# Optimization experiments

Hardware: AMD Instinct MI355X
Metric: run time of the kernel (lower is better)

The kernel has to match this reference:

```python
import jax, jax.numpy as jnp
import numpy as np

B, H, S, D = 4, 8, 8192, 64


def setup_inputs() -> dict:
    key = jax.random.key(0)
    kq, kk, kv_, kqm, kkm = jax.random.split(key, 5)
    q = jax.random.normal(kq, (B, H, S, D), dtype=jnp.float32)
    k = jax.random.normal(kk, (B, H, S, D), dtype=jnp.float32)
    v = jax.random.normal(kv_, (B, H, S, D), dtype=jnp.float32)
    q_mask = jax.random.randint(kqm, (B, S), 0, 2).astype(jnp.bool_)
    kv_mask = jax.random.randint(kkm, (B, S), 0, 2).astype(jnp.bool_)
    return {"q": q, "k": k, "v": v, "q_mask": q_mask, "kv_mask": kv_mask}


def reference(q, k, v, q_mask, kv_mask):
    # Linear (kernelized) attention branch: feature map phi(x) = elu(x) + 1
    qe = jax.nn.elu(q) + 1.0
    ke = jax.nn.elu(k) + 1.0
    qm = q_mask.astype(q.dtype)[:, None, :, None]   # [B,1,S,1]
    km = kv_mask.astype(q.dtype)[:, None, :, None]
    qe = qe * qm
    ke = ke * km
    ve = v * km
    s = v.shape[2]
    # kv: [B,H,D,D] contraction over kv sequence
    kv = jnp.einsum('bhsd,bhsc->bhdc', ke, ve / s)
    # normalizer per query position: [B,H,L]
    div = 1.0 / (jnp.einsum('bhld,bhsd->bhl', qe, ke) + 1e-6)
    out = s * jnp.einsum('bhld,bhdc,bhl->bhlc', qe, kv, div)
    return out
```

## Files before the change

kernel.cpp:

```cpp
#include <hip/hip_runtime.h>
#include <hip/hip_bf16.h>


#define S_LEN 8192
#define NBH 32
#define KVSTRIDE 4160

typedef __attribute__((ext_vector_type(8))) short short8;
typedef __attribute__((ext_vector_type(4))) float f32x4;

__device__ __forceinline__ float elu1(float x) {
  return x > 0.0f ? (x + 1.0f) : __expf(x);
}
__device__ __forceinline__ unsigned short f2bf(float x) {
  __hip_bfloat16 h = __float2bfloat16(x);
  union { __hip_bfloat16 b; unsigned short u; } cv; cv.b = h; return cv.u;
}
__device__ __forceinline__ float bf2f(unsigned short u) {
  return __uint_as_float(((unsigned)u) << 16);
}
__device__ __forceinline__ void split2(float x, unsigned short& hi, unsigned short& lo) {
  hi = f2bf(x);
  lo = f2bf(x - bf2f(hi));
}
__device__ __forceinline__ short8 ones8() {
  short8 o;
#pragma unroll
  for (int i = 0; i < 8; ++i) o[i] = (short)0x3F80;
  return o;
}

#define MFMA(a,b,c) __builtin_amdgcn_mfma_f32_16x16x32_bf16((a),(b),(c),0,0,0)

__global__ __launch_bounds__(256) void k1_partial(
    const float* __restrict__ kin, const float* __restrict__ vin,
    const int* __restrict__ kv_mask, float* __restrict__ partials, int seg_rows) {
  __shared__ unsigned short keT_h[64 * 72];
  __shared__ unsigned short keT_l[64 * 72];
  __shared__ unsigned short veT_h[64 * 72];
  __shared__ unsigned short veT_l[64 * 72];
  const int tid = threadIdx.x;
  const int seg = blockIdx.x, bh = blockIdx.y, b = bh >> 3;
  const int dp = tid & 31;
  const int so = tid >> 5;
  const int lane = tid & 63, w = tid >> 6;
  const int mrow = lane & 15, qd4 = lane >> 4;
  const short8 one = ones8();

  f32x4 acc[4]; f32x4 accs;
#pragma unroll
  for (int t = 0; t < 4; ++t) acc[t] = (f32x4){0.f, 0.f, 0.f, 0.f};
  accs = (f32x4){0.f, 0.f, 0.f, 0.f};

  const int rbase = seg * seg_rows;
  for (int t0 = 0; t0 < seg_rows; t0 += 64) {
    const int r0 = rbase + t0;
    const float* kp = kin + ((size_t)bh * S_LEN + r0 + so * 8) * 64 + dp * 2;
    const float* vp = vin + ((size_t)bh * S_LEN + r0 + so * 8) * 64 + dp * 2;
    union { unsigned short u[8]; uint4 v; } kh0, kh1, kl0, kl1, vh0, vh1, vl0, vl1;
#pragma unroll
    for (int r = 0; r < 8; ++r) {
      float m = kv_mask[b * S_LEN + r0 + so * 8 + r] ? 1.0f : 0.0f;
      float2 kw = *(const float2*)(kp + (size_t)r * 64);
      float2 vw = *(const float2*)(vp + (size_t)r * 64);
      float ka = elu1(kw.x) * m;
      float kb = elu1(kw.y) * m;
      float mv = m * (1.0f / 8192.0f);
      float va = vw.x * mv, vb = vw.y * mv;
      split2(ka, kh0.u[r], kl0.u[r]);
      split2(kb, kh1.u[r], kl1.u[r]);
      split2(va, vh0.u[r], vl0.u[r]);
      split2(vb, vh1.u[r], vl1.u[r]);
    }
    const int d0 = dp * 2;
    *(uint4*)&keT_h[(d0    ) * 72 + so * 8] = kh0.v;
    *(uint4*)&keT_h[(d0 + 1) * 72 + so * 8] = kh1.v;
    *(uint4*)&keT_l[(d0    ) * 72 + so * 8] = kl0.v;
    *(uint4*)&keT_l[(d0 + 1) * 72 + so * 8] = kl1.v;
    *(uint4*)&veT_h[(d0    ) * 72 + so * 8] = vh0.v;
    *(uint4*)&veT_h[(d0 + 1) * 72 + so * 8] = vh1.v;
    *(uint4*)&veT_l[(d0    ) * 72 + so * 8] = vl0.v;
    *(uint4*)&veT_l[(d0 + 1) * 72 + so * 8] = vl1.v;
    __syncthreads();
#pragma unroll
    for (int k0 = 0; k0 < 64; k0 += 32) {
      short8 a_h = *(const short8*)&keT_h[(w * 16 + mrow) * 72 + k0 + qd4 * 8];
      short8 a_l = *(const short8*)&keT_l[(w * 16 + mrow) * 72 + k0 + qd4 * 8];
      accs = MFMA(a_h, one, accs);
      accs = MFMA(a_l, one, accs);
#pragma unroll
      for (int t = 0; t < 4; ++t) {
        short8 b_h = *(const short8*)&veT_h[(t * 16 + mrow) * 72 + k0 + qd4 * 8];
        short8 b_l = *(const short8*)&veT_l[(t * 16 + mrow) * 72 + k0 + qd4 * 8];
        acc[t] = MFMA(a_h, b_h, acc[t]);
        acc[t] = MFMA(a_h, b_l, acc[t]);
        acc[t] = MFMA(a_l, b_h, acc[t]);
      }
    }
    __syncthreads();
  }
  float* p = partials + ((size_t)bh * gridDim.x + seg) * KVSTRIDE;
#pragma unroll
  for (int t = 0; t < 4; ++t)
#pragma unroll
    for (int r = 0; r < 4; ++r)
      p[(w * 16 + qd4 * 4 + r) * 64 + t * 16 + mrow] = acc[t][r];
  if (mrow == 0) {
#pragma unroll
    for (int r = 0; r < 4; ++r) p[4096 + w * 16 + qd4 * 4 + r] = accs[r];
  }
}

__global__ __launch_bounds__(256) void k2_reduce(
    const float* __restrict__ partials,
    unsigned short* __restrict__ kvTh, unsigned short* __restrict__ kvTl,
    unsigned short* __restrict__ ksh, unsigned short* __restrict__ ksl, int nchunk) {
  const int idx = blockIdx.x * 256 + threadIdx.x;
  if (idx >= NBH * KVSTRIDE) return;
  const int bh = idx / KVSTRIDE;
  const int e = idx - bh * KVSTRIDE;
  const float* p = partials + (size_t)bh * nchunk * KVSTRIDE + e;
  float s0 = 0.f, s1 = 0.f, s2 = 0.f, s3 = 0.f;
  int c = 0;
  for (; c + 4 <= nchunk; c += 4) {
    s0 += p[(size_t)(c + 0) * KVSTRIDE];
    s1 += p[(size_t)(c + 1) * KVSTRIDE];
    s2 += p[(size_t)(c + 2) * KVSTRIDE];
    s3 += p[(size_t)(c + 3) * KVSTRIDE];
  }
  for (; c < nchunk; ++c) s0 += p[(size_t)c * KVSTRIDE];
  float s = (s0 + s1) + (s2 + s3);
  unsigned short hi, lo;
  split2(s, hi, lo);
  if (e < 4096) {
    int d = e >> 6, cc = e & 63;
    kvTh[(size_t)bh * 4096 + cc * 64 + d] = hi;
    kvTl[(size_t)bh * 4096 + cc * 64 + d] = lo;
  } else {
    int d = e - 4096;
    ksh[bh * 64 + d] = hi;
    ksl[bh * 64 + d] = lo;
  }
}

__global__ __launch_bounds__(256) void k3_out(
    const float* __restrict__ qin, const int* __restrict__ q_mask,
    const unsigned short* __restrict__ kvTh_g, const unsigned short* __restrict__ kvTl_g,
    const unsigned short* __restrict__ ksh_g, const unsigned short* __restrict__ ksl_g,
    float* __restrict__ out) {
  __shared__ unsigned short qe_h[64 * 72];
  __shared__ unsigned short qe_l[64 * 72];
  __shared__ unsigned short kv_h[64 * 72];
  __shared__ unsigned short kv_l[64 * 72];
  __shared__ __align__(16) unsigned short ks_h[64];
  __shared__ __align__(16) unsigned short ks_l[64];
  const int tid = threadIdx.x;
  const int rb = blockIdx.x, bh = blockIdx.y, b = bh >> 3;
  const int r0 = rb * 64;
#pragma unroll
  for (int i = 0; i < 4; ++i) {
    int qd = i * 256 + tid;
    int l = qd >> 4, dq = qd & 15;
    float m = q_mask[b * S_LEN + r0 + l] ? 1.0f : 0.0f;
    float4 qw = *(const float4*)(qin + ((size_t)bh * S_LEN + r0 + l) * 64 + dq * 4);
    union { unsigned short u[4]; uint2 v; } h, lo;
    float e0 = elu1(qw.x) * m, e1 = elu1(qw.y) * m, e2 = elu1(qw.z) * m, e3 = elu1(qw.w) * m;
    split2(e0, h.u[0], lo.u[0]);
    split2(e1, h.u[1], lo.u[1]);
    split2(e2, h.u[2], lo.u[2]);
    split2(e3, h.u[3], lo.u[3]);
    *(uint2*)&qe_h[l * 72 + dq * 4] = h.v;
    *(uint2*)&qe_l[l * 72 + dq * 4] = lo.v;
  }
  for (int e = tid; e < 2048; e += 256) {
    int c = (e * 2) >> 6, d = (e * 2) & 63;
    *(unsigned*)&kv_h[c * 72 + d] = *(const unsigned*)(kvTh_g + (size_t)bh * 4096 + e * 2);
    *(unsigned*)&kv_l[c * 72 + d] = *(const unsigned*)(kvTl_g + (size_t)bh * 4096 + e * 2);
  }
  if (tid < 64) {
    ks_h[tid] = ksh_g[bh * 64 + tid];
    ks_l[tid] = ksl_g[bh * 64 + tid];
  }
  __syncthreads();
  const int lane = tid & 63, w = tid >> 6;
  const int mrow = lane & 15, qd4 = lane >> 4;
  f32x4 acc[4]; f32x4 accd;
#pragma unroll
  for (int t = 0; t < 4; ++t) acc[t] = (f32x4){0.f, 0.f, 0.f, 0.f};
  accd = (f32x4){0.f, 0.f, 0.f, 0.f};
#pragma unroll
  for (int k0 = 0; k0 < 64; k0 += 32) {
    short8 a_h = *(const short8*)&qe_h[(w * 16 + mrow) * 72 + k0 + qd4 * 8];
    short8 a_l = *(const short8*)&qe_l[(w * 16 + mrow) * 72 + k0 + qd4 * 8];
    short8 s_h = *(const short8*)&ks_h[k0 + qd4 * 8];
    short8 s_l = *(const short8*)&ks_l[k0 + qd4 * 8];
    accd = MFMA(a_h, s_h, accd);
    accd = MFMA(a_h, s_l, accd);
    accd = MFMA(a_l, s_h, accd);
#pragma unroll
    for (int t = 0; t < 4; ++t) {
      short8 b_h = *(const short8*)&kv_h[(t * 16 + mrow) * 72 + k0 + qd4 * 8];
      short8 b_l = *(const short8*)&kv_l[(t * 16 + mrow) * 72 + k0 + qd4 * 8];
      acc[t] = MFMA(a_h, b_h, acc[t]);
      acc[t] = MFMA(a_h, b_l, acc[t]);
      acc[t] = MFMA(a_l, b_h, acc[t]);
    }
  }
#pragma unroll
  for (int r = 0; r < 4; ++r) {
    float inv = 8192.0f / (accd[r] + 1e-6f);
    int row = r0 + w * 16 + qd4 * 4 + r;
#pragma unroll
    for (int t = 0; t < 4; ++t)
      out[((size_t)bh * S_LEN + row) * 64 + t * 16 + mrow] = acc[t][r] * inv;
  }
}

extern "C" void kernel_launch(void* const* d_in, const int* in_sizes, int n_in,
                              void* d_out, int out_size, void* d_ws, size_t ws_size,
                              hipStream_t stream) {
  const float* q = (const float*)d_in[0];
  const float* k = (const float*)d_in[1];
  const float* v = (const float*)d_in[2];
  const int* qm = (const int*)d_in[3];
  const int* km = (const int*)d_in[4];
  float* out = (float*)d_out;

  int nchunk = 32;
  while (nchunk > 1) {
    size_t need = (size_t)NBH * nchunk * KVSTRIDE * 4
                + (size_t)NBH * 4096 * 2 * 2 + (size_t)NBH * 64 * 2 * 2;
    if (need <= ws_size) break;
    nchunk >>= 1;
  }
  float* partials = (float*)d_ws;
  unsigned short* kvTh = (unsigned short*)(partials + (size_t)NBH * nchunk * KVSTRIDE);
  unsigned short* kvTl = kvTh + (size_t)NBH * 4096;
  unsigned short* ksh  = kvTl + (size_t)NBH * 4096;
  unsigned short* ksl  = ksh + NBH * 64;
  int seg_rows = S_LEN / nchunk;

  k1_partial<<<dim3(nchunk, NBH), 256, 0, stream>>>(k, v, km, partials, seg_rows);
  int n_elem = NBH * KVSTRIDE;
  k2_reduce<<<dim3((n_elem + 255) / 256), 256, 0, stream>>>(partials, kvTh, kvTl, ksh, ksl, nchunk);
  k3_out<<<dim3(S_LEN / 64, NBH), 256, 0, stream>>>(q, qm, kvTh, kvTl, ksh, ksl, out);
}
```

Before: 240.4 us.

## Replace split-bf16 MFMA path with fp32 FMA and register double-buffered loads

The three-way bf16 hi/lo split MFMA emulation of fp32 is dropped in all kernels and replaced by plain fp32 FMA outer products on LDS tiles. k1 gains register double buffering of K/V tiles, computes the key sum with per-thread vector adds, and doubles the chunk count. k2 now writes plain fp32 kv. k3 computes the normalizer with a dot product and an LDS reduction. This removes the conversion and split work and the 3x MFMA count, but the matmuls now run on the vector ALUs instead of the matrix cores.

```diff
diff --git a/kernel.cpp b/kernel.cpp
--- a/kernel.cpp
+++ b/kernel.cpp
@@ -1,120 +1,125 @@
 #include <hip/hip_runtime.h>
-#include <hip/hip_bf16.h>
 
 
 #define S_LEN 8192
 #define NBH 32
 #define KVSTRIDE 4160
 
-typedef __attribute__((ext_vector_type(8))) short short8;
 typedef __attribute__((ext_vector_type(4))) float f32x4;
 
 __device__ __forceinline__ float elu1(float x) {
   return x > 0.0f ? (x + 1.0f) : __expf(x);
 }
-__device__ __forceinline__ unsigned short f2bf(float x) {
-  __hip_bfloat16 h = __float2bfloat16(x);
-  union { __hip_bfloat16 b; unsigned short u; } cv; cv.b = h; return cv.u;
-}
-__device__ __forceinline__ float bf2f(unsigned short u) {
-  return __uint_as_float(((unsigned)u) << 16);
-}
-__device__ __forceinline__ void split2(float x, unsigned short& hi, unsigned short& lo) {
-  hi = f2bf(x);
-  lo = f2bf(x - bf2f(hi));
-}
-__device__ __forceinline__ short8 ones8() {
-  short8 o;
-#pragma unroll
-  for (int i = 0; i < 8; ++i) o[i] = (short)0x3F80;
-  return o;
-}
-
-#define MFMA(a,b,c) __builtin_amdgcn_mfma_f32_16x16x32_bf16((a),(b),(c),0,0,0)
 
 __global__ __launch_bounds__(256) void k1_partial(
     const float* __restrict__ kin, const float* __restrict__ vin,
     const int* __restrict__ kv_mask, float* __restrict__ partials, int seg_rows) {
-  __shared__ unsigned short keT_h[64 * 72];
-  __shared__ unsigned short keT_l[64 * 72];
-  __shared__ unsigned short veT_h[64 * 72];
-  __shared__ unsigned short veT_l[64 * 72];
+  __shared__ float ke_lds[64 * 64];
+  __shared__ float ve_lds[64 * 64];
   const int tid = threadIdx.x;
   const int seg = blockIdx.x, bh = blockIdx.y, b = bh >> 3;
-  const int dp = tid & 31;
-  const int so = tid >> 5;
-  const int lane = tid & 63, w = tid >> 6;
-  const int mrow = lane & 15, qd4 = lane >> 4;
-  const short8 one = ones8();
-
-  f32x4 acc[4]; f32x4 accs;
-#pragma unroll
-  for (int t = 0; t < 4; ++t) acc[t] = (f32x4){0.f, 0.f, 0.f, 0.f};
-  accs = (f32x4){0.f, 0.f, 0.f, 0.f};
-
   const int rbase = seg * seg_rows;
-  for (int t0 = 0; t0 < seg_rows; t0 += 64) {
-    const int r0 = rbase + t0;
-    const float* kp = kin + ((size_t)bh * S_LEN + r0 + so * 8) * 64 + dp * 2;
-    const float* vp = vin + ((size_t)bh * S_LEN + r0 + so * 8) * 64 + dp * 2;
-    union { unsigned short u[8]; uint4 v; } kh0, kh1, kl0, kl1, vh0, vh1, vl0, vl1;
-#pragma unroll
-    for (int r = 0; r < 8; ++r) {
-      float m = kv_mask[b * S_LEN + r0 + so * 8 + r] ? 1.0f : 0.0f;
-      float2 kw = *(const float2*)(kp + (size_t)r * 64);
-      float2 vw = *(const float2*)(vp + (size_t)r * 64);
-      float ka = elu1(kw.x) * m;
-      float kb = elu1(kw.y) * m;
-      float mv = m * (1.0f / 8192.0f);
-      float va = vw.x * mv, vb = vw.y * mv;
-      split2(ka, kh0.u[r], kl0.u[r]);
-      split2(kb, kh1.u[r], kl1.u[r]);
-      split2(va, vh0.u[r], vl0.u[r]);
-      split2(vb, vh1.u[r], vl1.u[r]);
-    }
-    const int d0 = dp * 2;
-    *(uint4*)&keT_h[(d0    ) * 72 + so * 8] = kh0.v;
-    *(uint4*)&keT_h[(d0 + 1) * 72 + so * 8] = kh1.v;
-    *(uint4*)&keT_l[(d0    ) * 72 + so * 8] = kl0.v;
-    *(uint4*)&keT_l[(d0 + 1) * 72 + so * 8] = kl1.v;
-    *(uint4*)&veT_h[(d0    ) * 72 + so * 8] = vh0.v;
-    *(uint4*)&veT_h[(d0 + 1) * 72 + so * 8] = vh1.v;
-    *(uint4*)&veT_l[(d0    ) * 72 + so * 8] = vl0.v;
-    *(uint4*)&veT_l[(d0 + 1) * 72 + so * 8] = vl1.v;
+  const int dg = tid >> 4, cg = tid & 15;
+  const float* kbase = kin + (size_t)bh * S_LEN * 64;
+  const float* vbase = vin + (size_t)bh * S_LEN * 64;
+  const int* mbase = kv_mask + b * S_LEN;
+
+  f32x4 ka[4], va[4], kb[4], vb[4];
+  float ma[4], mb[4];
+  float acc[4][4];
+#pragma unroll
+  for (int i = 0; i < 4; ++i)
+#pragma unroll
+    for (int j = 0; j < 4; ++j) acc[i][j] = 0.f;
+  f32x4 ksump = {0.f, 0.f, 0.f, 0.f};
+
+#define LOAD_T(K, V, M, r0_)                                           \
+  {                                                                    \
+    const float* kp_ = kbase + (size_t)(r0_) * 64;                     \
+    const float* vp_ = vbase + (size_t)(r0_) * 64;                     \
+    _Pragma("unroll")                                                  \
+    for (int i_ = 0; i_ < 4; ++i_) {                                   \
+      int f_ = tid + 256 * i_;                                         \
+      K[i_] = *(const f32x4*)(kp_ + (size_t)f_ * 4);                   \
+      V[i_] = *(const f32x4*)(vp_ + (size_t)f_ * 4);                   \
+      M[i_] = mbase[(r0_) + (tid >> 4) + 16 * i_] ? 1.0f : 0.0f;       \
+    }                                                                  \
+  }
+
+#define STORE_T(K, V, M)                                               \
+  {                                                                    \
+    _Pragma("unroll")                                                  \
+    for (int i_ = 0; i_ < 4; ++i_) {                                   \
+      int row_ = (tid >> 4) + 16 * i_;                                 \
+      int c4_ = (tid & 15) * 4;                                        \
+      float m_ = M[i_];                                                \
+      float mv_ = m_ * (1.0f / 8192.0f);                               \
+      f32x4 ke4_, ve4_;                                                \
+      _Pragma("unroll")                                                \
+      for (int j_ = 0; j_ < 4; ++j_) {                                 \
+        ke4_[j_] = elu1(K[i_][j_]) * m_;                               \
+        ve4_[j_] = V[i_][j_] * mv_;                                    \
+      }                                                                \
+      ksump += ke4_;      \
+      *(f32x4*)&ke_lds[row_ * 64 + c4_] = ke4_;                        \
+      *(f32x4*)&ve_lds[row_ * 64 + c4_] = ve4_;                        \
+    }                                                                  \
+  }
+
+#define COMPUTE_T()                                                    \
+  {                                                                    \
+    _Pragma("unroll 4")                                                \
+    for (int s_ = 0; s_ < 64; ++s_) {                                  \
+      f32x4 kd_ = *(const f32x4*)&ke_lds[s_ * 64 + dg * 4];            \
+      f32x4 vc_ = *(const f32x4*)&ve_lds[s_ * 64 + cg * 4];            \
+      _Pragma("unroll")                                                \
+      for (int i_ = 0; i_ < 4; ++i_)                                   \
+        _Pragma("unroll")                                              \
+        for (int j_ = 0; j_ < 4; ++j_)                                 \
+          acc[i_][j_] = fmaf(kd_[i_], vc_[j_], acc[i_][j_]);           \
+    }                                                                  \
+  }
+
+  const int ntiles = seg_rows >> 6;
+  LOAD_T(ka, va, ma, rbase)
+  for (int t = 0; t < ntiles; t += 2) {
+    if (t) __syncthreads();
+    STORE_T(ka, va, ma)
+    LOAD_T(kb, vb, mb, rbase + (t + 1) * 64)
     __syncthreads();
-#pragma unroll
-    for (int k0 = 0; k0 < 64; k0 += 32) {
-      short8 a_h = *(const short8*)&keT_h[(w * 16 + mrow) * 72 + k0 + qd4 * 8];
-      short8 a_l = *(const short8*)&keT_l[(w * 16 + mrow) * 72 + k0 + qd4 * 8];
-      accs = MFMA(a_h, one, accs);
-      accs = MFMA(a_l, one, accs);
-#pragma unroll
-      for (int t = 0; t < 4; ++t) {
-        short8 b_h = *(const short8*)&veT_h[(t * 16 + mrow) * 72 + k0 + qd4 * 8];
-        short8 b_l = *(const short8*)&veT_l[(t * 16 + mrow) * 72 + k0 + qd4 * 8];
-        acc[t] = MFMA(a_h, b_h, acc[t]);
-        acc[t] = MFMA(a_h, b_l, acc[t]);
-        acc[t] = MFMA(a_l, b_h, acc[t]);
-      }
-    }
+    COMPUTE_T()
     __syncthreads();
-  }
+    STORE_T(kb, vb, mb)
+    if (t + 2 < ntiles) LOAD_T(ka, va, ma, rbase + (t + 2) * 64)
+    __syncthreads();
+    COMPUTE_T()
+  }
+
   float* p = partials + ((size_t)bh * gridDim.x + seg) * KVSTRIDE;
 #pragma unroll
-  for (int t = 0; t < 4; ++t)
-#pragma unroll
-    for (int r = 0; r < 4; ++r)
-      p[(w * 16 + qd4 * 4 + r) * 64 + t * 16 + mrow] = acc[t][r];
-  if (mrow == 0) {
-#pragma unroll
-    for (int r = 0; r < 4; ++r) p[4096 + w * 16 + qd4 * 4 + r] = accs[r];
-  }
+  for (int i = 0; i < 4; ++i) {
+    f32x4 o;
+#pragma unroll
+    for (int j = 0; j < 4; ++j) o[j] = acc[i][j];
+    *(f32x4*)&p[(dg * 4 + i) * 64 + cg * 4] = o;
+  }
+  __syncthreads();
+  *(f32x4*)&ke_lds[tid * 4] = ksump;
+  __syncthreads();
+  if (tid < 64) {
+    float s = 0.f;
+#pragma unroll
+    for (int g = 0; g < 16; ++g)
+      s += ke_lds[(g * 16 + (tid >> 2)) * 4 + (tid & 3)];
+    p[4096 + tid] = s;
+  }
+#undef LOAD_T
+#undef STORE_T
+#undef COMPUTE_T
 }
 
 __global__ __launch_bounds__(256) void k2_reduce(
-    const float* __restrict__ partials,
-    unsigned short* __restrict__ kvTh, unsigned short* __restrict__ kvTl,
-    unsigned short* __restrict__ ksh, unsigned short* __restrict__ ksl, int nchunk) {
+    const float* __restrict__ partials, float* __restrict__ kvg, int nchunk) {
   const int idx = blockIdx.x * 256 + threadIdx.x;
   if (idx >= NBH * KVSTRIDE) return;
   const int bh = idx / KVSTRIDE;
@@ -129,90 +134,79 @@
     s3 += p[(size_t)(c + 3) * KVSTRIDE];
   }
   for (; c < nchunk; ++c) s0 += p[(size_t)c * KVSTRIDE];
-  float s = (s0 + s1) + (s2 + s3);
-  unsigned short hi, lo;
-  split2(s, hi, lo);
-  if (e < 4096) {
-    int d = e >> 6, cc = e & 63;
-    kvTh[(size_t)bh * 4096 + cc * 64 + d] = hi;
-    kvTl[(size_t)bh * 4096 + cc * 64 + d] = lo;
-  } else {
-    int d = e - 4096;
-    ksh[bh * 64 + d] = hi;
-    ksl[bh * 64 + d] = lo;
-  }
+  kvg[idx] = (s0 + s1) + (s2 + s3);
 }
 
 __global__ __launch_bounds__(256) void k3_out(
     const float* __restrict__ qin, const int* __restrict__ q_mask,
-    const unsigned short* __restrict__ kvTh_g, const unsigned short* __restrict__ kvTl_g,
-    const unsigned short* __restrict__ ksh_g, const unsigned short* __restrict__ ksl_g,
-    float* __restrict__ out) {
-  __shared__ unsigned short qe_h[64 * 72];
-  __shared__ unsigned short qe_l[64 * 72];
-  __shared__ unsigned short kv_h[64 * 72];
-  __shared__ unsigned short kv_l[64 * 72];
-  __shared__ __align__(16) unsigned short ks_h[64];
-  __shared__ __align__(16) unsigned short ks_l[64];
+    const float* __restrict__ kvg, float* __restrict__ out) {
+  __shared__ float qe_lds[64 * 66];
+  __shared__ float kv_lds[64 * 64];
+  __shared__ float den_lds[256 * 4];
+  __shared__ float inv_lds[64];
   const int tid = threadIdx.x;
   const int rb = blockIdx.x, bh = blockIdx.y, b = bh >> 3;
   const int r0 = rb * 64;
+  const int lg = tid >> 4, cg = tid & 15;
+  const float* kvb = kvg + (size_t)bh * KVSTRIDE;
+  const f32x4 ks4 = *(const f32x4*)(kvb + 4096 + cg * 4);
+  const float* qb = qin + ((size_t)bh * S_LEN + r0) * 64;
+
+  f32x4 denp;
 #pragma unroll
   for (int i = 0; i < 4; ++i) {
-    int qd = i * 256 + tid;
-    int l = qd >> 4, dq = qd & 15;
-    float m = q_mask[b * S_LEN + r0 + l] ? 1.0f : 0.0f;
-    float4 qw = *(const float4*)(qin + ((size_t)bh * S_LEN + r0 + l) * 64 + dq * 4);
-    union { unsigned short u[4]; uint2 v; } h, lo;
-    float e0 = elu1(qw.x) * m, e1 = elu1(qw.y) * m, e2 = elu1(qw.z) * m, e3 = elu1(qw.w) * m;
-    split2(e0, h.u[0], lo.u[0]);
-    split2(e1, h.u[1], lo.u[1]);
-    split2(e2, h.u[2], lo.u[2]);
-    split2(e3, h.u[3], lo.u[3]);
-    *(uint2*)&qe_h[l * 72 + dq * 4] = h.v;
-    *(uint2*)&qe_l[l * 72 + dq * 4] = lo.v;
-  }
-  for (int e = tid; e < 2048; e += 256) {
-    int c = (e * 2) >> 6, d = (e * 2) & 63;
-    *(unsigned*)&kv_h[c * 72 + d] = *(const unsigned*)(kvTh_g + (size_t)bh * 4096 + e * 2);
-    *(unsigned*)&kv_l[c * 72 + d] = *(const unsigned*)(kvTl_g + (size_t)bh * 4096 + e * 2);
-  }
+    int f = tid + 256 * i;
+    int row = (tid >> 4) + 16 * i, c4 = cg * 4;
+    float m = q_mask[b * S_LEN + r0 + row] ? 1.0f : 0.0f;
+    f32x4 qw = *(const f32x4*)(qb + (size_t)f * 4);
+    f32x4 qe;
+#pragma unroll
+    for (int j = 0; j < 4; ++j) qe[j] = elu1(qw[j]) * m;
+    *(f32x4*)&qe_lds[row * 66 + c4] = qe;
+    denp[i] = qe[0] * ks4[0] + qe[1] * ks4[1] + qe[2] * ks4[2] + qe[3] * ks4[3];
+    *(f32x4*)&kv_lds[f * 4] = *(const f32x4*)(kvb + (size_t)f * 4);
+  }
+  *(f32x4*)&den_lds[tid * 4] = denp;
+  __syncthreads();
   if (tid < 64) {
-    ks_h[tid] = ksh_g[bh * 64 + tid];
-    ks_l[tid] = ksl_g[bh * 64 + tid];
-  }
-  __syncthreads();
-  const int lane = tid & 63, w = tid >> 6;
-  const int mrow = lane & 15, qd4 = lane >> 4;
-  f32x4 acc[4]; f32x4 accd;
-#pragma unroll
-  for (int t = 0; t < 4; ++t) acc[t] = (f32x4){0.f, 0.f, 0.f, 0.f};
-  accd = (f32x4){0.f, 0.f, 0.f, 0.f};
-#pragma unroll
-  for (int k0 = 0; k0 < 64; k0 += 32) {
-    short8 a_h = *(const short8*)&qe_h[(w * 16 + mrow) * 72 + k0 + qd4 * 8];
-    short8 a_l = *(const short8*)&qe_l[(w * 16 + mrow) * 72 + k0 + qd4 * 8];
-    short8 s_h = *(const short8*)&ks_h[k0 + qd4 * 8];
-    short8 s_l = *(const short8*)&ks_l[k0 + qd4 * 8];
-    accd = MFMA(a_h, s_h, accd);
-    accd = MFMA(a_h, s_l, accd);
-    accd = MFMA(a_l, s_h, accd);
-#pragma unroll
-    for (int t = 0; t < 4; ++t) {
-      short8 b_h = *(const short8*)&kv_h[(t * 16 + mrow) * 72 + k0 + qd4 * 8];
-      short8 b_l = *(const short8*)&kv_l[(t * 16 + mrow) * 72 + k0 + qd4 * 8];
-      acc[t] = MFMA(a_h, b_h, acc[t]);
-      acc[t] = MFMA(a_h, b_l, acc[t]);
-      acc[t] = MFMA(a_l, b_h, acc[t]);
+    float s = 0.f;
+#pragma unroll
+    for (int g = 0; g < 16; ++g)
+      s += den_lds[((tid & 15) * 16 + g) * 4 + (tid >> 4)];
+    inv_lds[tid] = 8192.0f / (s + 1e-6f);
+  }
+
+  float acc[4][4];
+#pragma unroll
+  for (int i = 0; i < 4; ++i)
+#pragma unroll
+    for (int j = 0; j < 4; ++j) acc[i][j] = 0.f;
+
+#pragma unroll 8
+  for (int d = 0; d < 64; d += 2) {
+    float2 qv0 = *(const float2*)&qe_lds[(lg * 4 + 0) * 66 + d];
+    float2 qv1 = *(const float2*)&qe_lds[(lg * 4 + 1) * 66 + d];
+    float2 qv2 = *(const float2*)&qe_lds[(lg * 4 + 2) * 66 + d];
+    float2 qv3 = *(const float2*)&qe_lds[(lg * 4 + 3) * 66 + d];
+    f32x4 kv0 = *(const f32x4*)&kv_lds[d * 64 + cg * 4];
+    f32x4 kv1 = *(const f32x4*)&kv_lds[(d + 1) * 64 + cg * 4];
+#pragma unroll
+    for (int j = 0; j < 4; ++j) {
+      acc[0][j] = fmaf(qv0.x, kv0[j], fmaf(qv0.y, kv1[j], acc[0][j]));
+      acc[1][j] = fmaf(qv1.x, kv0[j], fmaf(qv1.y, kv1[j], acc[1][j]));
+      acc[2][j] = fmaf(qv2.x, kv0[j], fmaf(qv2.y, kv1[j], acc[2][j]));
+      acc[3][j] = fmaf(qv3.x, kv0[j], fmaf(qv3.y, kv1[j], acc[3][j]));
     }
   }
-#pragma unroll
-  for (int r = 0; r < 4; ++r) {
-    float inv = 8192.0f / (accd[r] + 1e-6f);
-    int row = r0 + w * 16 + qd4 * 4 + r;
-#pragma unroll
-    for (int t = 0; t < 4; ++t)
-      out[((size_t)bh * S_LEN + row) * 64 + t * 16 + mrow] = acc[t][r] * inv;
+  __syncthreads();
+#pragma unroll
+  for (int il = 0; il < 4; ++il) {
+    int row = lg * 4 + il;
+    float inv = inv_lds[row];
+    f32x4 o;
+#pragma unroll
+    for (int j = 0; j < 4; ++j) o[j] = acc[il][j] * inv;
+    *(f32x4*)(out + ((size_t)bh * S_LEN + r0 + row) * 64 + cg * 4) = o;
   }
 }
 
@@ -226,22 +220,18 @@
   const int* km = (const int*)d_in[4];
   float* out = (float*)d_out;
 
-  int nchunk = 32;
+  int nchunk = 64;
   while (nchunk > 1) {
-    size_t need = (size_t)NBH * nchunk * KVSTRIDE * 4
-                + (size_t)NBH * 4096 * 2 * 2 + (size_t)NBH * 64 * 2 * 2;
+    size_t need = (size_t)NBH * nchunk * KVSTRIDE * 4 + (size_t)NBH * KVSTRIDE * 4;
     if (need <= ws_size) break;
     nchunk >>= 1;
   }
   float* partials = (float*)d_ws;
-  unsigned short* kvTh = (unsigned short*)(partials + (size_t)NBH * nchunk * KVSTRIDE);
-  unsigned short* kvTl = kvTh + (size_t)NBH * 4096;
-  unsigned short* ksh  = kvTl + (size_t)NBH * 4096;
-  unsigned short* ksl  = ksh + NBH * 64;
+  float* kvg = partials + (size_t)NBH * nchunk * KVSTRIDE;
   int seg_rows = S_LEN / nchunk;
 
   k1_partial<<<dim3(nchunk, NBH), 256, 0, stream>>>(k, v, km, partials, seg_rows);
   int n_elem = NBH * KVSTRIDE;
-  k2_reduce<<<dim3((n_elem + 255) / 256), 256, 0, stream>>>(partials, kvTh, kvTl, ksh, ksl, nchunk);
-  k3_out<<<dim3(S_LEN / 64, NBH), 256, 0, stream>>>(q, qm, kvTh, kvTl, ksh, ksl, out);
-}
+  k2_reduce<<<dim3((n_elem + 255) / 256), 256, 0, stream>>>(partials, kvg, nchunk);
+  k3_out<<<dim3(S_LEN / 64, NBH), 256, 0, stream>>>(q, qm, kvg, out);
+}
```

Result: no change. 242.9 us (+1.1%).
